# Kernel optimization log

Measured on AMD Instinct MI355X. Metric: run time of the kernel, lower is better.

Reference implementation:

```python
import jax, jax.numpy as jnp
import numpy as np

B, T, V, E, U = 1024, 128, 32000, 128, 512


def setup_inputs() -> dict:
    key = jax.random.key(0)
    ks = jax.random.split(key, 8)
    s = lambda k, *sh: jax.random.normal(k, sh, dtype=jnp.float32) * 0.05
    return {
        "tokens": jax.random.randint(ks[0], (B, T), 0, V, dtype=jnp.int32),
        "emb": s(ks[1], V, E),
        "Wx0": s(ks[2], E, U),
        "Wh0": s(ks[3], U, U),
        "b0": jnp.zeros((U,), jnp.float32),
        "Wx1": s(ks[4], U, U),
        "Wh1": s(ks[5], U, U),
        "b1": jnp.zeros((U,), jnp.float32),
        "Wo": s(ks[6], U, 1),
        "bo": jnp.zeros((1,), jnp.float32),
    }


def reference(tokens, emb, Wx0, Wh0, b0, Wx1, Wh1, b1, Wo, bo):
    # Embedding lookup: [B, T, E]
    x = emb[tokens]
    xs = jnp.swapaxes(x, 0, 1)  # [T, B, E] for time-major scan
    h0 = jnp.zeros((tokens.shape[0], Wh0.shape[0]), x.dtype)
    h1 = jnp.zeros((tokens.shape[0], Wh1.shape[0]), x.dtype)

    def step(carry, xt):
        h0, h1 = carry
        # SimpleRNNCell layer 0: h' = tanh(x@Wx + h@Wh + b)
        h0 = jnp.tanh(xt @ Wx0 + h0 @ Wh0 + b0)
        # SimpleRNNCell layer 1 stacked on out0
        h1 = jnp.tanh(h0 @ Wx1 + h1 @ Wh1 + b1)
        return (h0, h1), None

    (h0, h1), _ = jax.lax.scan(step, (h0, h1), xs)
    logits = h1 @ Wo + bo            # [B, 1]
    return jax.nn.sigmoid(logits)
```

## Files before the change

### kernel.cpp

```cpp
#include <hip/hip_runtime.h>
#include <hip/hip_bf16.h>

#define B_ 1024
#define T_ 128
#define E_ 128
#define U_ 512
#define V_ 32000
#define NC 16
#define NG 16
#define MB 64
#define NB 32
#define HS ((size_t)B_ * U_)

#define CTR_OFF 0
#define XMASK_OFF (512u << 10)
#define FH0_OFF (520u << 10)
#define FH1_OFF (528u << 10)
#define H0H_OFF (1u << 20)
#define H0L_OFF (4u << 20)
#define H1H_OFF (7u << 20)
#define H1L_OFF (9u << 20)
#define EMBW_OFF (11u << 20)
#define ZERO_BYTES (11u << 20)

typedef unsigned int uint32;
typedef __bf16 bf16x8 __attribute__((ext_vector_type(8)));
typedef float f32x4 __attribute__((ext_vector_type(4)));
typedef unsigned short us8 __attribute__((ext_vector_type(8)));

#define MFMA __builtin_amdgcn_mfma_f32_16x16x32_bf16

__device__ __forceinline__ unsigned short f2b(float f) {
  uint32 u = __builtin_bit_cast(uint32, f);
  u += 0x7fffu + ((u >> 16) & 1u);
  return (unsigned short)(u >> 16);
}
__device__ __forceinline__ float b2f(unsigned short h) {
  return __builtin_bit_cast(float, (uint32)h << 16);
}

__device__ __forceinline__ bf16x8 lds_frag(const unsigned short* s, int row, int k, int K) {
  uint32 off = (uint32)((row * K + k) * 2) ^ (uint32)((row & 7) << 4);
  us8 v = *(const us8*)((const char*)s + off);
  return __builtin_bit_cast(bf16x8, v);
}
__device__ __forceinline__ bf16x8 g_frag(const unsigned short* p) {
  us8 v = *(const us8*)p;
  return __builtin_bit_cast(bf16x8, v);
}
__device__ __forceinline__ void st_coh(unsigned short* p, unsigned short v) {
  __hip_atomic_store(p, v, __ATOMIC_RELAXED, __HIP_MEMORY_SCOPE_AGENT);
}
template <bool FAST>
__device__ __forceinline__ void st_h(unsigned short* p, unsigned short v) {
  if (FAST) *p = v; else st_coh(p, v);
}

template <bool FAST>
__device__ __forceinline__ void wave_signal(uint32* f, uint32 val, int lane) {
  asm volatile("s_waitcnt vmcnt(0)" ::: "memory");
  if (lane == 0) {
    if (FAST) *(volatile uint32*)f = val;
    else __hip_atomic_store(f, val, __ATOMIC_RELAXED, __HIP_MEMORY_SCOPE_AGENT);
  }
}

template <bool FAST, int DLT>
__device__ __forceinline__ void wave_wait(const uint32* f0, const uint32* f1,
                                          int t, int lane) {
  if (t == 0) return;
  const int t1 = t - DLT;
  const uint32 tgt = (lane < 16) ? (uint32)t
                                 : ((lane < 32 && t1 > 0) ? (uint32)t1 : 0u);
  const uint32* p = (lane < 16) ? (f0 + lane)
                                : ((lane < 32) ? (f1 + (lane & 15)) : f0);
  while (true) {
    uint32 v;
    if (FAST) v = *(const volatile uint32*)p;
    else v = __hip_atomic_load(p, __ATOMIC_RELAXED, __HIP_MEMORY_SCOPE_AGENT);
    if (__all(v >= tgt)) break;
    if (FAST) asm volatile("buffer_inv" ::: "memory");
    __builtin_amdgcn_s_sleep(2);
  }
  if (FAST) asm volatile("buffer_inv\n\ts_waitcnt vmcnt(0)" ::: "memory");
  else __builtin_amdgcn_fence(__ATOMIC_ACQUIRE, "agent");
}

__device__ __forceinline__ void bar_agent(uint32* ctr, int phase, int g, int tid) {
  asm volatile("s_waitcnt vmcnt(0)" ::: "memory");
  __syncthreads();
  if (tid == 0) {
    uint32* a = &ctr[(uint32)((phase << 4) | g) << 4];
    __hip_atomic_fetch_add(a, 1u, __ATOMIC_RELAXED, __HIP_MEMORY_SCOPE_AGENT);
    while (__hip_atomic_load(a, __ATOMIC_RELAXED, __HIP_MEMORY_SCOPE_AGENT) < NC)
      __builtin_amdgcn_s_sleep(1);
    __builtin_amdgcn_fence(__ATOMIC_ACQUIRE, "agent");
  }
  __syncthreads();
}

__global__ void rnn_init(unsigned char* ws) {
  const uint4 z = {0u, 0u, 0u, 0u};
  uint4* p = (uint4*)ws;
  size_t n = ZERO_BYTES / 16;
  for (size_t j = (size_t)blockIdx.x * blockDim.x + threadIdx.x; j < n;
       j += (size_t)gridDim.x * blockDim.x)
    p[j] = z;
}

__global__ __launch_bounds__(256) void embw_gemm(const float* __restrict__ emb,
                                                 const float* __restrict__ Wx0,
                                                 unsigned short* __restrict__ embW) {
  const int tid = threadIdx.x;
  const int lane = tid & 63;
  const int wv = tid >> 6;
  const int arow = lane & 15;
  const int kgrp = (lane >> 4) * 8;
  const int vrow = blockIdx.x * 64 + wv * 16;

  bf16x8 a[4];
  for (int kt = 0; kt < 4; ++kt) {
    const float* p = emb + (size_t)(vrow + arow) * E_ + kt * 32 + kgrp;
    float4 f0 = ((const float4*)p)[0];
    float4 f1 = ((const float4*)p)[1];
    us8 u;
    u[0] = f2b(f0.x); u[1] = f2b(f0.y); u[2] = f2b(f0.z); u[3] = f2b(f0.w);
    u[4] = f2b(f1.x); u[5] = f2b(f1.y); u[6] = f2b(f1.z); u[7] = f2b(f1.w);
    a[kt] = __builtin_bit_cast(bf16x8, u);
  }
  const int c0 = blockIdx.y * 64;
  for (int nt = 0; nt < 4; ++nt) {
    const int col = c0 + nt * 16 + (lane & 15);
    f32x4 acc = {0.f, 0.f, 0.f, 0.f};
    for (int kt = 0; kt < 4; ++kt) {
      us8 ub;
      for (int j = 0; j < 8; ++j)
        ub[j] = f2b(Wx0[(size_t)(kt * 32 + kgrp + j) * U_ + col]);
      acc = MFMA(a[kt], __builtin_bit_cast(bf16x8, ub), acc, 0, 0, 0);
    }
    const int crow = vrow + (lane >> 4) * 4;
    for (int i = 0; i < 4; ++i)
      embW[(size_t)(crow + i) * U_ + col] = f2b(acc[i]);
  }
}

template <bool FAST>
__device__ __forceinline__ void l0_loop(
    const int* __restrict__ tokens, const unsigned short* __restrict__ embW,
    unsigned short* h0h, unsigned short* h0l, const uint32* f0w,
    const uint32* f1w, uint32* myF0, const unsigned short* sWh0h,
    const unsigned short* sWh0l, int r0, int c0, int lane, int rowB, int kgrp,
    int rowA, float b0v0, float b0v1) {
  const int l15 = lane & 15;
  const float b0a[2] = {b0v0, b0v1};
  unsigned short embP[2][4];
#pragma unroll
  for (int nt = 0; nt < 2; ++nt)
    for (int i = 0; i < 4; ++i) {
      int tk = tokens[(size_t)(r0 + rowB + i) * T_ + 0];
      embP[nt][i] = embW[(size_t)tk * U_ + c0 + nt * 16 + l15];
    }

  for (int t = 0; t < T_; ++t) {
    wave_wait<FAST, 2>(f0w, f1w, t, lane);

    const size_t rb = (size_t)((t + 2) % 3) * HS;
    bf16x8 hh[16], hl[16];
    {
      const unsigned short* ph = h0h + rb + (size_t)rowA * U_ + kgrp;
      const unsigned short* pl = h0l + rb + (size_t)rowA * U_ + kgrp;
#pragma unroll
      for (int kt = 0; kt < 16; ++kt) {
        hh[kt] = g_frag(ph + kt * 32);
        hl[kt] = g_frag(pl + kt * 32);
      }
    }
    const size_t wb = (size_t)(t % 3) * HS;
#pragma unroll
    for (int nt = 0; nt < 2; ++nt) {
      const int colL = nt * 16 + l15;
      f32x4 aC, aD = {0.f, 0.f, 0.f, 0.f};
      for (int i = 0; i < 4; ++i) aC[i] = b0a[nt] + b2f(embP[nt][i]);
#pragma unroll
      for (int kt = 0; kt < 16; ++kt) {
        bf16x8 bh = lds_frag(sWh0h, colL, kt * 32 + kgrp, U_);
        bf16x8 bl = lds_frag(sWh0l, colL, kt * 32 + kgrp, U_);
        aC = MFMA(hh[kt], bh, aC, 0, 0, 0);
        aD = MFMA(hl[kt], bh, aD, 0, 0, 0);
        aD = MFMA(hh[kt], bl, aD, 0, 0, 0);
      }
      size_t ob = wb + (size_t)(r0 + rowB) * U_ + (c0 + colL);
      for (int i = 0; i < 4; ++i) {
        float v = tanhf(aC[i] + aD[i]);
        unsigned short hi = f2b(v);
        st_h<FAST>(&h0h[ob + (size_t)i * U_], hi);
        st_h<FAST>(&h0l[ob + (size_t)i * U_], f2b(v - b2f(hi)));
      }
    }
    wave_signal<FAST>(myF0, (uint32)(t + 1), lane);

    if (t + 1 < T_) {
#pragma unroll
      for (int nt = 0; nt < 2; ++nt)
        for (int i = 0; i < 4; ++i) {
          int tk = tokens[(size_t)(r0 + rowB + i) * T_ + (t + 1)];
          embP[nt][i] = embW[(size_t)tk * U_ + c0 + nt * 16 + l15];
        }
    }
  }
}

template <bool FAST>
__device__ __forceinline__ void l1_loop(
    unsigned short* h0h, unsigned short* h0l, unsigned short* h1h,
    unsigned short* h1l, const uint32* f0w, const uint32* f1w, uint32* myF1,
    const unsigned short* sWx1h, const unsigned short* sWh1h,
    const unsigned short* sWh1l, int r0, int c0, int lane, int rowB, int kgrp,
    int rowA, float b1v0, float b1v1) {
  const int l15 = lane & 15;
  const float b1a[2] = {b1v0, b1v1};

  for (int w = 1; w <= T_; ++w) {
    wave_wait<FAST, 1>(f0w, f1w, w, lane);

    f32x4 aB[2];
    {
      const size_t rb1 = (size_t)(w & 1) * HS;
      bf16x8 ah[16], al[16];
      const unsigned short* p1h = h1h + rb1 + (size_t)rowA * U_ + kgrp;
      const unsigned short* p1l = h1l + rb1 + (size_t)rowA * U_ + kgrp;
#pragma unroll
      for (int kt = 0; kt < 16; ++kt) {
        ah[kt] = g_frag(p1h + kt * 32);
        al[kt] = g_frag(p1l + kt * 32);
      }
#pragma unroll
      for (int nt = 0; nt < 2; ++nt) {
        const int colL = nt * 16 + l15;
        f32x4 acc = {b1a[nt], b1a[nt], b1a[nt], b1a[nt]};
#pragma unroll
        for (int kt = 0; kt < 16; ++kt) {
          bf16x8 bh = lds_frag(sWh1h, colL, kt * 32 + kgrp, U_);
          acc = MFMA(ah[kt], bh, acc, 0, 0, 0);
          acc = MFMA(al[kt], bh, acc, 0, 0, 0);
          if (kt < 15) {
            bf16x8 bl = lds_frag(sWh1l, colL, kt * 32 + kgrp, 480);
            acc = MFMA(ah[kt], bl, acc, 0, 0, 0);
          }
        }
        aB[nt] = acc;
      }
    }
    const size_t rb0 = (size_t)((w + 2) % 3) * HS;
    bf16x8 hh[16], hl[16];
    {
      const unsigned short* ph = h0h + rb0 + (size_t)rowA * U_ + kgrp;
      const unsigned short* pl = h0l + rb0 + (size_t)rowA * U_ + kgrp;
#pragma unroll
      for (int kt = 0; kt < 16; ++kt) {
        hh[kt] = g_frag(ph + kt * 32);
        hl[kt] = g_frag(pl + kt * 32);
      }
    }
    const size_t wb1 = (size_t)((w - 1) & 1) * HS;
#pragma unroll
    for (int nt = 0; nt < 2; ++nt) {
      const int colL = nt * 16 + l15;
      f32x4 aA = {0.f, 0.f, 0.f, 0.f};
#pragma unroll
      for (int kt = 0; kt < 16; ++kt) {
        bf16x8 bxh = lds_frag(sWx1h, colL, kt * 32 + kgrp, U_);
        aA = MFMA(hh[kt], bxh, aA, 0, 0, 0);
        aA = MFMA(hl[kt], bxh, aA, 0, 0, 0);
      }
      size_t ob = wb1 + (size_t)(r0 + rowB) * U_ + (c0 + colL);
      for (int i = 0; i < 4; ++i) {
        float v = tanhf(aA[i] + aB[nt][i]);
        unsigned short hi = f2b(v);
        st_h<FAST>(&h1h[ob + (size_t)i * U_], hi);
        st_h<FAST>(&h1l[ob + (size_t)i * U_], f2b(v - b2f(hi)));
      }
    }
    wave_signal<FAST>(myF1, (uint32)w, lane);
  }
}

__global__ __launch_bounds__(512, 2) void rnn_main(
    const int* __restrict__ tokens, const float* __restrict__ b0,
    const float* __restrict__ Wh0, const float* __restrict__ Wx1,
    const float* __restrict__ Wh1, const float* __restrict__ b1,
    unsigned char* ws) {
  __shared__ unsigned short sWh0h[NB * U_];
  __shared__ unsigned short sWh0l[NB * U_];
  __shared__ unsigned short sWx1h[NB * U_];
  __shared__ unsigned short sWh1h[NB * U_];
  __shared__ unsigned short sWh1l[NB * 480];
  __shared__ uint32 sFast;

  const int tid = threadIdx.x;
  const int bid = blockIdx.x;
  const int g = bid & (NG - 1);
  const int c = bid >> 4;
  const int r0 = g * MB;
  const int c0 = c * NB;

  uint32* ctr = (uint32*)(ws + CTR_OFF);
  uint32* fH0 = (uint32*)(ws + FH0_OFF);
  uint32* fH1 = (uint32*)(ws + FH1_OFF);
  unsigned short* h0h = (unsigned short*)(ws + H0H_OFF);
  unsigned short* h0l = (unsigned short*)(ws + H0L_OFF);
  unsigned short* h1h = (unsigned short*)(ws + H1H_OFF);
  unsigned short* h1l = (unsigned short*)(ws + H1L_OFF);
  const unsigned short* embW = (const unsigned short*)(ws + EMBW_OFF);

  for (int idx = tid; idx < NB * U_; idx += 512) {
    int cl = idx & 31, k = idx >> 5;
    float v = Wh0[(size_t)k * U_ + c0 + cl];
    unsigned short hi = f2b(v);
    uint32 off = (uint32)((cl * U_ + k) * 2) ^ (uint32)((cl & 7) << 4);
    *(unsigned short*)((char*)sWh0h + off) = hi;
    *(unsigned short*)((char*)sWh0l + off) = f2b(v - b2f(hi));
  }
  for (int idx = tid; idx < NB * U_; idx += 512) {
    int cl = idx & 31, k = idx >> 5;
    float v = Wx1[(size_t)k * U_ + c0 + cl];
    uint32 off = (uint32)((cl * U_ + k) * 2) ^ (uint32)((cl & 7) << 4);
    *(unsigned short*)((char*)sWx1h + off) = f2b(v);
  }
  for (int idx = tid; idx < NB * U_; idx += 512) {
    int cl = idx & 31, k = idx >> 5;
    float v = Wh1[(size_t)k * U_ + c0 + cl];
    unsigned short hi = f2b(v);
    uint32 off = (uint32)((cl * U_ + k) * 2) ^ (uint32)((cl & 7) << 4);
    *(unsigned short*)((char*)sWh1h + off) = hi;
    if (k < 480) {
      uint32 offl = (uint32)((cl * 480 + k) * 2) ^ (uint32)((cl & 7) << 4);
      *(unsigned short*)((char*)sWh1l + offl) = f2b(v - b2f(hi));
    }
  }

  {
    uint32 xcd;
    asm volatile("s_getreg_b32 %0, hwreg(HW_REG_XCC_ID)" : "=s"(xcd));
    uint32* xm = (uint32*)(ws + XMASK_OFF) + (uint32)g * 16;
    if (tid == 0)
      __hip_atomic_fetch_or(xm, 1u << (xcd & 31u), __ATOMIC_RELAXED,
                            __HIP_MEMORY_SCOPE_AGENT);
    bar_agent(ctr, T_, g, tid);
    if (tid == 0) {
      uint32 m = __hip_atomic_load(xm, __ATOMIC_RELAXED, __HIP_MEMORY_SCOPE_AGENT);
      sFast = (__popc(m) == 1) ? 1u : 0u;
    }
  }

  const int lane = tid & 63;
  const int wv = tid >> 6;
  const int mt = wv & 3;
  const int role = wv >> 2;
  const int l15 = lane & 15;
  const int rowB = mt * 16 + ((lane >> 4) << 2);
  const int kgrp = (lane >> 4) * 8;
  const int rowA = r0 + mt * 16 + l15;

  const uint32* f0w = fH0 + (((uint32)g * 4 + mt) << 4);
  const uint32* f1w = fH1 + (((uint32)g * 4 + mt) << 4);
  uint32* myF0 = (uint32*)f0w + c;
  uint32* myF1 = (uint32*)f1w + c;

  __syncthreads();
  const bool fast = (sFast != 0);

  if (role == 0) {
    const float b0v0 = b0[c0 + l15], b0v1 = b0[c0 + 16 + l15];
    if (fast)
      l0_loop<true>(tokens, embW, h0h, h0l, f0w, f1w, myF0, sWh0h, sWh0l, r0,
                    c0, lane, rowB, kgrp, rowA, b0v0, b0v1);
    else
      l0_loop<false>(tokens, embW, h0h, h0l, f0w, f1w, myF0, sWh0h, sWh0l, r0,
                     c0, lane, rowB, kgrp, rowA, b0v0, b0v1);
  } else {
    const float b1v0 = b1[c0 + l15], b1v1 = b1[c0 + 16 + l15];
    if (fast)
      l1_loop<true>(h0h, h0l, h1h, h1l, f0w, f1w, myF1, sWx1h, sWh1h, sWh1l,
                    r0, c0, lane, rowB, kgrp, rowA, b1v0, b1v1);
    else
      l1_loop<false>(h0h, h0l, h1h, h1l, f0w, f1w, myF1, sWx1h, sWh1h, sWh1l,
                     r0, c0, lane, rowB, kgrp, rowA, b1v0, b1v1);
  }
}

__global__ void rnn_final(const unsigned short* __restrict__ h1h,
                          const unsigned short* __restrict__ h1l,
                          const float* __restrict__ Wo,
                          const float* __restrict__ bo, float* __restrict__ out) {
  int lane = threadIdx.x & 63;
  int b = blockIdx.x * 4 + (threadIdx.x >> 6);
  us8 hh = *(const us8*)(h1h + (size_t)b * U_ + lane * 8);
  us8 hl = *(const us8*)(h1l + (size_t)b * U_ + lane * 8);
  const float4* wp = (const float4*)(Wo + lane * 8);
  float4 w0 = wp[0], w1 = wp[1];
  float s = (b2f(hh[0]) + b2f(hl[0])) * w0.x + (b2f(hh[1]) + b2f(hl[1])) * w0.y +
            (b2f(hh[2]) + b2f(hl[2])) * w0.z + (b2f(hh[3]) + b2f(hl[3])) * w0.w +
            (b2f(hh[4]) + b2f(hl[4])) * w1.x + (b2f(hh[5]) + b2f(hl[5])) * w1.y +
            (b2f(hh[6]) + b2f(hl[6])) * w1.z + (b2f(hh[7]) + b2f(hl[7])) * w1.w;
  for (int off = 32; off > 0; off >>= 1) s += __shfl_down(s, off, 64);
  if (lane == 0) out[b] = 1.0f / (1.0f + expf(-(s + bo[0])));
}

extern "C" void kernel_launch(void* const* d_in, const int* in_sizes, int n_in,
                              void* d_out, int out_size, void* d_ws, size_t ws_size,
                              hipStream_t stream) {
  const int* tokens = (const int*)d_in[0];
  const float* emb = (const float*)d_in[1];
  const float* Wx0 = (const float*)d_in[2];
  const float* Wh0 = (const float*)d_in[3];
  const float* b0 = (const float*)d_in[4];
  const float* Wx1 = (const float*)d_in[5];
  const float* Wh1 = (const float*)d_in[6];
  const float* b1 = (const float*)d_in[7];
  const float* Wo = (const float*)d_in[8];
  const float* bo = (const float*)d_in[9];
  unsigned char* ws = (unsigned char*)d_ws;
  float* out = (float*)d_out;

  hipLaunchKernelGGL(rnn_init, dim3(1024), dim3(256), 0, stream, ws);
  hipLaunchKernelGGL(embw_gemm, dim3(V_ / 64, U_ / 64), dim3(256), 0, stream,
                     emb, Wx0, (unsigned short*)(ws + EMBW_OFF));
  hipLaunchKernelGGL(rnn_main, dim3(NC * NG), dim3(512), 0, stream, tokens,
                     b0, Wh0, Wx1, Wh1, b1, ws);
  hipLaunchKernelGGL(rnn_final, dim3(256), dim3(256), 0, stream,
                     (const unsigned short*)(ws + H1H_OFF) + (size_t)1 * B_ * U_,
                     (const unsigned short*)(ws + H1L_OFF) + (size_t)1 * B_ * U_,
                     Wo, bo, out);
}
```

Before: 2.576 ms.

## Merge layer roles into per-column waves sharing h0 fragments across layers

The kernel used to give each wave either the layer-0 role or the layer-1 role, each covering two 16-column tiles. Now every wave handles one 16-column tile for both layers. It computes the h0 recurrence and the Wx1 projection from the same loaded h0 fragments, then runs the layer-1 step for the previous timestep. This avoids loading the h0 fragments twice and changes the flag layout to 32 per-wave flags, with separate pollers for layer 0 and layer 1. In exchange, layer 1 is now serialized inside the same wave, so the earlier overlap between layer-0 and layer-1 waves is lost, and each wave does more polling per step.

Result: faster. 2.313 ms (-10.2%).

```diff
diff --git a/kernel.cpp b/kernel.cpp
--- a/kernel.cpp
+++ b/kernel.cpp
@@ -57,23 +57,8 @@
 }
 
 template <bool FAST>
-__device__ __forceinline__ void wave_signal(uint32* f, uint32 val, int lane) {
-  asm volatile("s_waitcnt vmcnt(0)" ::: "memory");
-  if (lane == 0) {
-    if (FAST) *(volatile uint32*)f = val;
-    else __hip_atomic_store(f, val, __ATOMIC_RELAXED, __HIP_MEMORY_SCOPE_AGENT);
-  }
-}
-
-template <bool FAST, int DLT>
-__device__ __forceinline__ void wave_wait(const uint32* f0, const uint32* f1,
-                                          int t, int lane) {
-  if (t == 0) return;
-  const int t1 = t - DLT;
-  const uint32 tgt = (lane < 16) ? (uint32)t
-                                 : ((lane < 32 && t1 > 0) ? (uint32)t1 : 0u);
-  const uint32* p = (lane < 16) ? (f0 + lane)
-                                : ((lane < 32) ? (f1 + (lane & 15)) : f0);
+__device__ __forceinline__ void poll32(const uint32* base, uint32 tgt, int lane) {
+  const uint32* p = base + (lane & 31);
   while (true) {
     uint32 v;
     if (FAST) v = *(const volatile uint32*)p;
@@ -84,6 +69,15 @@
   }
   if (FAST) asm volatile("buffer_inv\n\ts_waitcnt vmcnt(0)" ::: "memory");
   else __builtin_amdgcn_fence(__ATOMIC_ACQUIRE, "agent");
+}
+
+template <bool FAST>
+__device__ __forceinline__ void signal(uint32* f, uint32 val, int lane) {
+  asm volatile("s_waitcnt vmcnt(0)" ::: "memory");
+  if (lane == 0) {
+    if (FAST) *(volatile uint32*)f = val;
+    else __hip_atomic_store(f, val, __ATOMIC_RELAXED, __HIP_MEMORY_SCOPE_AGENT);
+  }
 }
 
 __device__ __forceinline__ void bar_agent(uint32* ctr, int phase, int g, int tid) {
@@ -145,50 +139,89 @@
 }
 
 template <bool FAST>
-__device__ __forceinline__ void l0_loop(
+__device__ __forceinline__ void l1_step(
+    int t, f32x4 aA, unsigned short* h1h, unsigned short* h1l,
+    const uint32* f1w, uint32* myF1, const unsigned short* sWh1h,
+    const unsigned short* sWh1l, int r0, int c0, int lane, int colL, int rowB,
+    int kgrp, int rowA, float b1v) {
+  poll32<FAST>(f1w, (uint32)(t - 1), lane);
+  const size_t rb1 = (size_t)(t & 1) * HS;
+  bf16x8 ah[16], al[16];
+  {
+    const unsigned short* p1h = h1h + rb1 + (size_t)rowA * U_ + kgrp;
+    const unsigned short* p1l = h1l + rb1 + (size_t)rowA * U_ + kgrp;
+#pragma unroll
+    for (int kt = 0; kt < 16; ++kt) {
+      ah[kt] = g_frag(p1h + kt * 32);
+      al[kt] = g_frag(p1l + kt * 32);
+    }
+  }
+  f32x4 aB = {b1v, b1v, b1v, b1v};
+#pragma unroll
+  for (int kt = 0; kt < 16; ++kt) {
+    bf16x8 wh = lds_frag(sWh1h, colL, kt * 32 + kgrp, U_);
+    aB = MFMA(ah[kt], wh, aB, 0, 0, 0);
+    aB = MFMA(al[kt], wh, aB, 0, 0, 0);
+    if (kt < 15) {
+      bf16x8 wl = lds_frag(sWh1l, colL, kt * 32 + kgrp, 480);
+      aB = MFMA(ah[kt], wl, aB, 0, 0, 0);
+    }
+  }
+  const size_t wb1 = (size_t)((t - 1) & 1) * HS;
+  size_t ob = wb1 + (size_t)(r0 + rowB) * U_ + (c0 + colL);
+  for (int i = 0; i < 4; ++i) {
+    float v = tanhf(aA[i] + aB[i]);
+    unsigned short hi = f2b(v);
+    st_h<FAST>(&h1h[ob + (size_t)i * U_], hi);
+    st_h<FAST>(&h1l[ob + (size_t)i * U_], f2b(v - b2f(hi)));
+  }
+  signal<FAST>(myF1, (uint32)t, lane);
+}
+
+template <bool FAST>
+__device__ __forceinline__ void rnn_wave(
     const int* __restrict__ tokens, const unsigned short* __restrict__ embW,
-    unsigned short* h0h, unsigned short* h0l, const uint32* f0w,
-    const uint32* f1w, uint32* myF0, const unsigned short* sWh0h,
-    const unsigned short* sWh0l, int r0, int c0, int lane, int rowB, int kgrp,
-    int rowA, float b0v0, float b0v1) {
-  const int l15 = lane & 15;
-  const float b0a[2] = {b0v0, b0v1};
-  unsigned short embP[2][4];
-#pragma unroll
-  for (int nt = 0; nt < 2; ++nt)
-    for (int i = 0; i < 4; ++i) {
-      int tk = tokens[(size_t)(r0 + rowB + i) * T_ + 0];
-      embP[nt][i] = embW[(size_t)tk * U_ + c0 + nt * 16 + l15];
-    }
+    unsigned short* h0h, unsigned short* h0l, unsigned short* h1h,
+    unsigned short* h1l, const uint32* f0w, const uint32* f1w, uint32* myF0,
+    uint32* myF1, const unsigned short* sWh0h, const unsigned short* sWh0l,
+    const unsigned short* sWx1h, const unsigned short* sWh1h,
+    const unsigned short* sWh1l, int r0, int c0, int lane, int colL, int rowB,
+    int kgrp, int rowA, float b0v, float b1v) {
+  unsigned short embP[4];
+  for (int i = 0; i < 4; ++i) {
+    int tk = tokens[(size_t)(r0 + rowB + i) * T_ + 0];
+    embP[i] = embW[(size_t)tk * U_ + c0 + colL];
+  }
 
   for (int t = 0; t < T_; ++t) {
-    wave_wait<FAST, 2>(f0w, f1w, t, lane);
-
-    const size_t rb = (size_t)((t + 2) % 3) * HS;
+    if (t > 0) poll32<FAST>(f0w, (uint32)t, lane);
+    const size_t rb0 = (size_t)((t + 2) % 3) * HS;
     bf16x8 hh[16], hl[16];
     {
-      const unsigned short* ph = h0h + rb + (size_t)rowA * U_ + kgrp;
-      const unsigned short* pl = h0l + rb + (size_t)rowA * U_ + kgrp;
+      const unsigned short* ph = h0h + rb0 + (size_t)rowA * U_ + kgrp;
+      const unsigned short* pl = h0l + rb0 + (size_t)rowA * U_ + kgrp;
 #pragma unroll
       for (int kt = 0; kt < 16; ++kt) {
         hh[kt] = g_frag(ph + kt * 32);
         hl[kt] = g_frag(pl + kt * 32);
       }
     }
-    const size_t wb = (size_t)(t % 3) * HS;
-#pragma unroll
-    for (int nt = 0; nt < 2; ++nt) {
-      const int colL = nt * 16 + l15;
-      f32x4 aC, aD = {0.f, 0.f, 0.f, 0.f};
-      for (int i = 0; i < 4; ++i) aC[i] = b0a[nt] + b2f(embP[nt][i]);
-#pragma unroll
-      for (int kt = 0; kt < 16; ++kt) {
-        bf16x8 bh = lds_frag(sWh0h, colL, kt * 32 + kgrp, U_);
-        bf16x8 bl = lds_frag(sWh0l, colL, kt * 32 + kgrp, U_);
-        aC = MFMA(hh[kt], bh, aC, 0, 0, 0);
-        aD = MFMA(hl[kt], bh, aD, 0, 0, 0);
-        aD = MFMA(hh[kt], bl, aD, 0, 0, 0);
-      }
+    f32x4 aA = {0.f, 0.f, 0.f, 0.f};
+    f32x4 aC, aD = {0.f, 0.f, 0.f, 0.f};
+    for (int i = 0; i < 4; ++i) aC[i] = b0v + b2f(embP[i]);
+#pragma unroll
+    for (int kt = 0; kt < 16; ++kt) {
+      bf16x8 wx = lds_frag(sWx1h, colL, kt * 32 + kgrp, U_);
+      bf16x8 wh = lds_frag(sWh0h, colL, kt * 32 + kgrp, U_);
+      bf16x8 wl = lds_frag(sWh0l, colL, kt * 32 + kgrp, U_);
+      aA = MFMA(hh[kt], wx, aA, 0, 0, 0);
+      aA = MFMA(hl[kt], wx, aA, 0, 0, 0);
+      aC = MFMA(hh[kt], wh, aC, 0, 0, 0);
+      aD = MFMA(hl[kt], wh, aD, 0, 0, 0);
+      aD = MFMA(hh[kt], wl, aD, 0, 0, 0);
+    }
+    {
+      const size_t wb = (size_t)(t % 3) * HS;
       size_t ob = wb + (size_t)(r0 + rowB) * U_ + (c0 + colL);
       for (int i = 0; i < 4; ++i) {
         float v = tanhf(aC[i] + aD[i]);
@@ -197,61 +230,23 @@
         st_h<FAST>(&h0l[ob + (size_t)i * U_], f2b(v - b2f(hi)));
       }
     }
-    wave_signal<FAST>(myF0, (uint32)(t + 1), lane);
+    signal<FAST>(myF0, (uint32)(t + 1), lane);
 
     if (t + 1 < T_) {
-#pragma unroll
-      for (int nt = 0; nt < 2; ++nt)
-        for (int i = 0; i < 4; ++i) {
-          int tk = tokens[(size_t)(r0 + rowB + i) * T_ + (t + 1)];
-          embP[nt][i] = embW[(size_t)tk * U_ + c0 + nt * 16 + l15];
-        }
-    }
-  }
-}
-
-template <bool FAST>
-__device__ __forceinline__ void l1_loop(
-    unsigned short* h0h, unsigned short* h0l, unsigned short* h1h,
-    unsigned short* h1l, const uint32* f0w, const uint32* f1w, uint32* myF1,
-    const unsigned short* sWx1h, const unsigned short* sWh1h,
-    const unsigned short* sWh1l, int r0, int c0, int lane, int rowB, int kgrp,
-    int rowA, float b1v0, float b1v1) {
-  const int l15 = lane & 15;
-  const float b1a[2] = {b1v0, b1v1};
-
-  for (int w = 1; w <= T_; ++w) {
-    wave_wait<FAST, 1>(f0w, f1w, w, lane);
-
-    f32x4 aB[2];
-    {
-      const size_t rb1 = (size_t)(w & 1) * HS;
-      bf16x8 ah[16], al[16];
-      const unsigned short* p1h = h1h + rb1 + (size_t)rowA * U_ + kgrp;
-      const unsigned short* p1l = h1l + rb1 + (size_t)rowA * U_ + kgrp;
-#pragma unroll
-      for (int kt = 0; kt < 16; ++kt) {
-        ah[kt] = g_frag(p1h + kt * 32);
-        al[kt] = g_frag(p1l + kt * 32);
+      for (int i = 0; i < 4; ++i) {
+        int tk = tokens[(size_t)(r0 + rowB + i) * T_ + (t + 1)];
+        embP[i] = embW[(size_t)tk * U_ + c0 + colL];
       }
-#pragma unroll
-      for (int nt = 0; nt < 2; ++nt) {
-        const int colL = nt * 16 + l15;
-        f32x4 acc = {b1a[nt], b1a[nt], b1a[nt], b1a[nt]};
-#pragma unroll
-        for (int kt = 0; kt < 16; ++kt) {
-          bf16x8 bh = lds_frag(sWh1h, colL, kt * 32 + kgrp, U_);
-          acc = MFMA(ah[kt], bh, acc, 0, 0, 0);
-          acc = MFMA(al[kt], bh, acc, 0, 0, 0);
-          if (kt < 15) {
-            bf16x8 bl = lds_frag(sWh1l, colL, kt * 32 + kgrp, 480);
-            acc = MFMA(ah[kt], bl, acc, 0, 0, 0);
-          }
-        }
-        aB[nt] = acc;
-      }
-    }
-    const size_t rb0 = (size_t)((w + 2) % 3) * HS;
+    }
+
+    if (t >= 1)
+      l1_step<FAST>(t, aA, h1h, h1l, f1w, myF1, sWh1h, sWh1l, r0, c0, lane,
+                    colL, rowB, kgrp, rowA, b1v);
+  }
+
+  {
+    poll32<FAST>(f0w, (uint32)T_, lane);
+    const size_t rb0 = (size_t)((T_ + 2) % 3) * HS;
     bf16x8 hh[16], hl[16];
     {
       const unsigned short* ph = h0h + rb0 + (size_t)rowA * U_ + kgrp;
@@ -262,26 +257,15 @@
         hl[kt] = g_frag(pl + kt * 32);
       }
     }
-    const size_t wb1 = (size_t)((w - 1) & 1) * HS;
-#pragma unroll
-    for (int nt = 0; nt < 2; ++nt) {
-      const int colL = nt * 16 + l15;
-      f32x4 aA = {0.f, 0.f, 0.f, 0.f};
-#pragma unroll
-      for (int kt = 0; kt < 16; ++kt) {
-        bf16x8 bxh = lds_frag(sWx1h, colL, kt * 32 + kgrp, U_);
-        aA = MFMA(hh[kt], bxh, aA, 0, 0, 0);
-        aA = MFMA(hl[kt], bxh, aA, 0, 0, 0);
-      }
-      size_t ob = wb1 + (size_t)(r0 + rowB) * U_ + (c0 + colL);
-      for (int i = 0; i < 4; ++i) {
-        float v = tanhf(aA[i] + aB[nt][i]);
-        unsigned short hi = f2b(v);
-        st_h<FAST>(&h1h[ob + (size_t)i * U_], hi);
-        st_h<FAST>(&h1l[ob + (size_t)i * U_], f2b(v - b2f(hi)));
-      }
-    }
-    wave_signal<FAST>(myF1, (uint32)w, lane);
+    f32x4 aA = {0.f, 0.f, 0.f, 0.f};
+#pragma unroll
+    for (int kt = 0; kt < 16; ++kt) {
+      bf16x8 wx = lds_frag(sWx1h, colL, kt * 32 + kgrp, U_);
+      aA = MFMA(hh[kt], wx, aA, 0, 0, 0);
+      aA = MFMA(hl[kt], wx, aA, 0, 0, 0);
+    }
+    l1_step<FAST>(T_, aA, h1h, h1l, f1w, myF1, sWh1h, sWh1l, r0, c0, lane,
+                  colL, rowB, kgrp, rowA, b1v);
   }
 }
 
@@ -356,37 +340,31 @@
   const int lane = tid & 63;
   const int wv = tid >> 6;
   const int mt = wv & 3;
-  const int role = wv >> 2;
+  const int nt = wv >> 2;
   const int l15 = lane & 15;
+  const int colL = nt * 16 + l15;
   const int rowB = mt * 16 + ((lane >> 4) << 2);
   const int kgrp = (lane >> 4) * 8;
   const int rowA = r0 + mt * 16 + l15;
-
-  const uint32* f0w = fH0 + (((uint32)g * 4 + mt) << 4);
-  const uint32* f1w = fH1 + (((uint32)g * 4 + mt) << 4);
-  uint32* myF0 = (uint32*)f0w + c;
-  uint32* myF1 = (uint32*)f1w + c;
+  const float b0v = b0[c0 + colL];
+  const float b1v = b1[c0 + colL];
+
+  const uint32* f0w = fH0 + ((uint32)(g * 4 + mt) * 32);
+  const uint32* f1w = fH1 + ((uint32)(g * 4 + mt) * 32);
+  uint32* myF0 = (uint32*)f0w + (c * 2 + nt);
+  uint32* myF1 = (uint32*)f1w + (c * 2 + nt);
 
   __syncthreads();
   const bool fast = (sFast != 0);
 
-  if (role == 0) {
-    const float b0v0 = b0[c0 + l15], b0v1 = b0[c0 + 16 + l15];
-    if (fast)
-      l0_loop<true>(tokens, embW, h0h, h0l, f0w, f1w, myF0, sWh0h, sWh0l, r0,
-                    c0, lane, rowB, kgrp, rowA, b0v0, b0v1);
-    else
-      l0_loop<false>(tokens, embW, h0h, h0l, f0w, f1w, myF0, sWh0h, sWh0l, r0,
-                     c0, lane, rowB, kgrp, rowA, b0v0, b0v1);
-  } else {
-    const float b1v0 = b1[c0 + l15], b1v1 = b1[c0 + 16 + l15];
-    if (fast)
-      l1_loop<true>(h0h, h0l, h1h, h1l, f0w, f1w, myF1, sWx1h, sWh1h, sWh1l,
-                    r0, c0, lane, rowB, kgrp, rowA, b1v0, b1v1);
-    else
-      l1_loop<false>(h0h, h0l, h1h, h1l, f0w, f1w, myF1, sWx1h, sWh1h, sWh1l,
-                     r0, c0, lane, rowB, kgrp, rowA, b1v0, b1v1);
-  }
+  if (fast)
+    rnn_wave<true>(tokens, embW, h0h, h0l, h1h, h1l, f0w, f1w, myF0, myF1,
+                   sWh0h, sWh0l, sWx1h, sWh1h, sWh1l, r0, c0, lane, colL,
+                   rowB, kgrp, rowA, b0v, b1v);
+  else
+    rnn_wave<false>(tokens, embW, h0h, h0l, h1h, h1l, f0w, f1w, myF0, myF1,
+                    sWh0h, sWh0l, sWx1h, sWh1h, sWh1l, r0, c0, lane, colL,
+                    rowB, kgrp, rowA, b0v, b1v);
 }
 
 __global__ void rnn_final(const unsigned short* __restrict__ h1h,
```

## Split each wave's two column tiles across separate waves with 1024-thread blocks

Applied to the files above, without the earlier changes.

Doubles the block to 1024 threads so each wave computes a single 16-column tile instead of two, halving the serial MFMA chain per wave inside the recurrent step. Per-wave progress flags grow from 16 to 32 per row group, and the poll now checks 32 layer-0 and 32 layer-1 flags across the full 64 lanes. This cuts per-step latency on the critical path. In exchange, each wave now reloads the full h fragments for only half the work, which doubles global reads of h per block, and the block loses the 2-blocks-per-CU launch bound.

Result: slower. 5.469 ms (+112.3%).

```diff
diff --git a/kernel.cpp b/kernel.cpp
--- a/kernel.cpp
+++ b/kernel.cpp
@@ -57,23 +57,12 @@
 }
 
 template <bool FAST>
-__device__ __forceinline__ void wave_signal(uint32* f, uint32 val, int lane) {
-  asm volatile("s_waitcnt vmcnt(0)" ::: "memory");
-  if (lane == 0) {
-    if (FAST) *(volatile uint32*)f = val;
-    else __hip_atomic_store(f, val, __ATOMIC_RELAXED, __HIP_MEMORY_SCOPE_AGENT);
-  }
-}
-
-template <bool FAST, int DLT>
-__device__ __forceinline__ void wave_wait(const uint32* f0, const uint32* f1,
-                                          int t, int lane) {
-  if (t == 0) return;
-  const int t1 = t - DLT;
-  const uint32 tgt = (lane < 16) ? (uint32)t
-                                 : ((lane < 32 && t1 > 0) ? (uint32)t1 : 0u);
-  const uint32* p = (lane < 16) ? (f0 + lane)
-                                : ((lane < 32) ? (f1 + (lane & 15)) : f0);
+__device__ __forceinline__ void poll64(const uint32* f0, const uint32* f1,
+                                       int t0, int t1, int lane) {
+  if (t0 <= 0 && t1 <= 0) return;
+  const uint32 tgt = (lane < 32) ? (uint32)(t0 > 0 ? t0 : 0)
+                                 : (uint32)(t1 > 0 ? t1 : 0);
+  const uint32* p = (lane < 32) ? (f0 + lane) : (f1 + (lane & 31));
   while (true) {
     uint32 v;
     if (FAST) v = *(const volatile uint32*)p;
@@ -84,6 +73,15 @@
   }
   if (FAST) asm volatile("buffer_inv\n\ts_waitcnt vmcnt(0)" ::: "memory");
   else __builtin_amdgcn_fence(__ATOMIC_ACQUIRE, "agent");
+}
+
+template <bool FAST>
+__device__ __forceinline__ void signal(uint32* f, uint32 val, int lane) {
+  asm volatile("s_waitcnt vmcnt(0)" ::: "memory");
+  if (lane == 0) {
+    if (FAST) *(volatile uint32*)f = val;
+    else __hip_atomic_store(f, val, __ATOMIC_RELAXED, __HIP_MEMORY_SCOPE_AGENT);
+  }
 }
 
 __device__ __forceinline__ void bar_agent(uint32* ctr, int phase, int g, int tid) {
@@ -149,20 +147,16 @@
     const int* __restrict__ tokens, const unsigned short* __restrict__ embW,
     unsigned short* h0h, unsigned short* h0l, const uint32* f0w,
     const uint32* f1w, uint32* myF0, const unsigned short* sWh0h,
-    const unsigned short* sWh0l, int r0, int c0, int lane, int rowB, int kgrp,
-    int rowA, float b0v0, float b0v1) {
-  const int l15 = lane & 15;
-  const float b0a[2] = {b0v0, b0v1};
-  unsigned short embP[2][4];
-#pragma unroll
-  for (int nt = 0; nt < 2; ++nt)
-    for (int i = 0; i < 4; ++i) {
-      int tk = tokens[(size_t)(r0 + rowB + i) * T_ + 0];
-      embP[nt][i] = embW[(size_t)tk * U_ + c0 + nt * 16 + l15];
-    }
+    const unsigned short* sWh0l, int r0, int c0, int lane, int colL, int rowB,
+    int kgrp, int rowA, float b0v) {
+  unsigned short embP[4];
+  for (int i = 0; i < 4; ++i) {
+    int tk = tokens[(size_t)(r0 + rowB + i) * T_ + 0];
+    embP[i] = embW[(size_t)tk * U_ + c0 + colL];
+  }
 
   for (int t = 0; t < T_; ++t) {
-    wave_wait<FAST, 2>(f0w, f1w, t, lane);
+    poll64<FAST>(f0w, f1w, t, t - 2, lane);
 
     const size_t rb = (size_t)((t + 2) % 3) * HS;
     bf16x8 hh[16], hl[16];
@@ -175,37 +169,31 @@
         hl[kt] = g_frag(pl + kt * 32);
       }
     }
+    f32x4 aC, aD = {0.f, 0.f, 0.f, 0.f};
+    for (int i = 0; i < 4; ++i) aC[i] = b0v + b2f(embP[i]);
+#pragma unroll
+    for (int kt = 0; kt < 16; ++kt) {
+      bf16x8 bh = lds_frag(sWh0h, colL, kt * 32 + kgrp, U_);
+      bf16x8 bl = lds_frag(sWh0l, colL, kt * 32 + kgrp, U_);
+      aC = MFMA(hh[kt], bh, aC, 0, 0, 0);
+      aD = MFMA(hl[kt], bh, aD, 0, 0, 0);
+      aD = MFMA(hh[kt], bl, aD, 0, 0, 0);
+    }
     const size_t wb = (size_t)(t % 3) * HS;
-#pragma unroll
-    for (int nt = 0; nt < 2; ++nt) {
-      const int colL = nt * 16 + l15;
-      f32x4 aC, aD = {0.f, 0.f, 0.f, 0.f};
-      for (int i = 0; i < 4; ++i) aC[i] = b0a[nt] + b2f(embP[nt][i]);
-#pragma unroll
-      for (int kt = 0; kt < 16; ++kt) {
-        bf16x8 bh = lds_frag(sWh0h, colL, kt * 32 + kgrp, U_);
-        bf16x8 bl = lds_frag(sWh0l, colL, kt * 32 + kgrp, U_);
-        aC = MFMA(hh[kt], bh, aC, 0, 0, 0);
-        aD = MFMA(hl[kt], bh, aD, 0, 0, 0);
-        aD = MFMA(hh[kt], bl, aD, 0, 0, 0);
-      }
-      size_t ob = wb + (size_t)(r0 + rowB) * U_ + (c0 + colL);
+    size_t ob = wb + (size_t)(r0 + rowB) * U_ + (c0 + colL);
+    for (int i = 0; i < 4; ++i) {
+      float v = tanhf(aC[i] + aD[i]);
+      unsigned short hi = f2b(v);
+      st_h<FAST>(&h0h[ob + (size_t)i * U_], hi);
+      st_h<FAST>(&h0l[ob + (size_t)i * U_], f2b(v - b2f(hi)));
+    }
+    signal<FAST>(myF0, (uint32)(t + 1), lane);
+
+    if (t + 1 < T_) {
       for (int i = 0; i < 4; ++i) {
-        float v = tanhf(aC[i] + aD[i]);
-        unsigned short hi = f2b(v);
-        st_h<FAST>(&h0h[ob + (size_t)i * U_], hi);
-        st_h<FAST>(&h0l[ob + (size_t)i * U_], f2b(v - b2f(hi)));
-      }
-    }
-    wave_signal<FAST>(myF0, (uint32)(t + 1), lane);
-
-    if (t + 1 < T_) {
-#pragma unroll
-      for (int nt = 0; nt < 2; ++nt)
-        for (int i = 0; i < 4; ++i) {
-          int tk = tokens[(size_t)(r0 + rowB + i) * T_ + (t + 1)];
-          embP[nt][i] = embW[(size_t)tk * U_ + c0 + nt * 16 + l15];
-        }
+        int tk = tokens[(size_t)(r0 + rowB + i) * T_ + (t + 1)];
+        embP[i] = embW[(size_t)tk * U_ + c0 + colL];
+      }
     }
   }
 }
@@ -215,15 +203,12 @@
     unsigned short* h0h, unsigned short* h0l, unsigned short* h1h,
     unsigned short* h1l, const uint32* f0w, const uint32* f1w, uint32* myF1,
     const unsigned short* sWx1h, const unsigned short* sWh1h,
-    const unsigned short* sWh1l, int r0, int c0, int lane, int rowB, int kgrp,
-    int rowA, float b1v0, float b1v1) {
-  const int l15 = lane & 15;
-  const float b1a[2] = {b1v0, b1v1};
-
+    const unsigned short* sWh1l, int r0, int c0, int lane, int colL, int rowB,
+    int kgrp, int rowA, float b1v) {
   for (int w = 1; w <= T_; ++w) {
-    wave_wait<FAST, 1>(f0w, f1w, w, lane);
-
-    f32x4 aB[2];
+    poll64<FAST>(f0w, f1w, w, w - 1, lane);
+
+    f32x4 aB = {b1v, b1v, b1v, b1v};
     {
       const size_t rb1 = (size_t)(w & 1) * HS;
       bf16x8 ah[16], al[16];
@@ -235,25 +220,20 @@
         al[kt] = g_frag(p1l + kt * 32);
       }
 #pragma unroll
-      for (int nt = 0; nt < 2; ++nt) {
-        const int colL = nt * 16 + l15;
-        f32x4 acc = {b1a[nt], b1a[nt], b1a[nt], b1a[nt]};
-#pragma unroll
-        for (int kt = 0; kt < 16; ++kt) {
-          bf16x8 bh = lds_frag(sWh1h, colL, kt * 32 + kgrp, U_);
-          acc = MFMA(ah[kt], bh, acc, 0, 0, 0);
-          acc = MFMA(al[kt], bh, acc, 0, 0, 0);
-          if (kt < 15) {
-            bf16x8 bl = lds_frag(sWh1l, colL, kt * 32 + kgrp, 480);
-            acc = MFMA(ah[kt], bl, acc, 0, 0, 0);
-          }
+      for (int kt = 0; kt < 16; ++kt) {
+        bf16x8 bh = lds_frag(sWh1h, colL, kt * 32 + kgrp, U_);
+        aB = MFMA(ah[kt], bh, aB, 0, 0, 0);
+        aB = MFMA(al[kt], bh, aB, 0, 0, 0);
+        if (kt < 15) {
+          bf16x8 bl = lds_frag(sWh1l, colL, kt * 32 + kgrp, 480);
+          aB = MFMA(ah[kt], bl, aB, 0, 0, 0);
         }
-        aB[nt] = acc;
-      }
-    }
-    const size_t rb0 = (size_t)((w + 2) % 3) * HS;
-    bf16x8 hh[16], hl[16];
+      }
+    }
+    f32x4 aA = {0.f, 0.f, 0.f, 0.f};
     {
+      const size_t rb0 = (size_t)((w + 2) % 3) * HS;
+      bf16x8 hh[16], hl[16];
       const unsigned short* ph = h0h + rb0 + (size_t)rowA * U_ + kgrp;
       const unsigned short* pl = h0l + rb0 + (size_t)rowA * U_ + kgrp;
 #pragma unroll
@@ -261,31 +241,26 @@
         hh[kt] = g_frag(ph + kt * 32);
         hl[kt] = g_frag(pl + kt * 32);
       }
-    }
-    const size_t wb1 = (size_t)((w - 1) & 1) * HS;
-#pragma unroll
-    for (int nt = 0; nt < 2; ++nt) {
-      const int colL = nt * 16 + l15;
-      f32x4 aA = {0.f, 0.f, 0.f, 0.f};
 #pragma unroll
       for (int kt = 0; kt < 16; ++kt) {
         bf16x8 bxh = lds_frag(sWx1h, colL, kt * 32 + kgrp, U_);
         aA = MFMA(hh[kt], bxh, aA, 0, 0, 0);
         aA = MFMA(hl[kt], bxh, aA, 0, 0, 0);
       }
-      size_t ob = wb1 + (size_t)(r0 + rowB) * U_ + (c0 + colL);
-      for (int i = 0; i < 4; ++i) {
-        float v = tanhf(aA[i] + aB[nt][i]);
-        unsigned short hi = f2b(v);
-        st_h<FAST>(&h1h[ob + (size_t)i * U_], hi);
-        st_h<FAST>(&h1l[ob + (size_t)i * U_], f2b(v - b2f(hi)));
-      }
-    }
-    wave_signal<FAST>(myF1, (uint32)w, lane);
-  }
-}
-
-__global__ __launch_bounds__(512, 2) void rnn_main(
+    }
+    const size_t wb1 = (size_t)((w - 1) & 1) * HS;
+    size_t ob = wb1 + (size_t)(r0 + rowB) * U_ + (c0 + colL);
+    for (int i = 0; i < 4; ++i) {
+      float v = tanhf(aA[i] + aB[i]);
+      unsigned short hi = f2b(v);
+      st_h<FAST>(&h1h[ob + (size_t)i * U_], hi);
+      st_h<FAST>(&h1l[ob + (size_t)i * U_], f2b(v - b2f(hi)));
+    }
+    signal<FAST>(myF1, (uint32)w, lane);
+  }
+}
+
+__global__ __launch_bounds__(1024) void rnn_main(
     const int* __restrict__ tokens, const float* __restrict__ b0,
     const float* __restrict__ Wh0, const float* __restrict__ Wx1,
     const float* __restrict__ Wh1, const float* __restrict__ b1,
@@ -313,7 +288,7 @@
   unsigned short* h1l = (unsigned short*)(ws + H1L_OFF);
   const unsigned short* embW = (const unsigned short*)(ws + EMBW_OFF);
 
-  for (int idx = tid; idx < NB * U_; idx += 512) {
+  for (int idx = tid; idx < NB * U_; idx += 1024) {
     int cl = idx & 31, k = idx >> 5;
     float v = Wh0[(size_t)k * U_ + c0 + cl];
     unsigned short hi = f2b(v);
@@ -321,13 +296,13 @@
     *(unsigned short*)((char*)sWh0h + off) = hi;
     *(unsigned short*)((char*)sWh0l + off) = f2b(v - b2f(hi));
   }
-  for (int idx = tid; idx < NB * U_; idx += 512) {
+  for (int idx = tid; idx < NB * U_; idx += 1024) {
     int cl = idx & 31, k = idx >> 5;
     float v = Wx1[(size_t)k * U_ + c0 + cl];
     uint32 off = (uint32)((cl * U_ + k) * 2) ^ (uint32)((cl & 7) << 4);
     *(unsigned short*)((char*)sWx1h + off) = f2b(v);
   }
-  for (int idx = tid; idx < NB * U_; idx += 512) {
+  for (int idx = tid; idx < NB * U_; idx += 1024) {
     int cl = idx & 31, k = idx >> 5;
     float v = Wh1[(size_t)k * U_ + c0 + cl];
     unsigned short hi = f2b(v);
@@ -356,36 +331,38 @@
   const int lane = tid & 63;
   const int wv = tid >> 6;
   const int mt = wv & 3;
-  const int role = wv >> 2;
+  const int nt = (wv >> 2) & 1;
+  const int role = wv >> 3;
   const int l15 = lane & 15;
+  const int colL = nt * 16 + l15;
   const int rowB = mt * 16 + ((lane >> 4) << 2);
   const int kgrp = (lane >> 4) * 8;
   const int rowA = r0 + mt * 16 + l15;
 
-  const uint32* f0w = fH0 + (((uint32)g * 4 + mt) << 4);
-  const uint32* f1w = fH1 + (((uint32)g * 4 + mt) << 4);
-  uint32* myF0 = (uint32*)f0w + c;
-  uint32* myF1 = (uint32*)f1w + c;
+  const uint32* f0w = fH0 + ((uint32)(g * 4 + mt) * 32);
+  const uint32* f1w = fH1 + ((uint32)(g * 4 + mt) * 32);
+  uint32* myF0 = (uint32*)f0w + (c * 2 + nt);
+  uint32* myF1 = (uint32*)f1w + (c * 2 + nt);
 
   __syncthreads();
   const bool fast = (sFast != 0);
 
   if (role == 0) {
-    const float b0v0 = b0[c0 + l15], b0v1 = b0[c0 + 16 + l15];
+    const float b0v = b0[c0 + colL];
     if (fast)
       l0_loop<true>(tokens, embW, h0h, h0l, f0w, f1w, myF0, sWh0h, sWh0l, r0,
-                    c0, lane, rowB, kgrp, rowA, b0v0, b0v1);
+                    c0, lane, colL, rowB, kgrp, rowA, b0v);
     else
       l0_loop<false>(tokens, embW, h0h, h0l, f0w, f1w, myF0, sWh0h, sWh0l, r0,
-                     c0, lane, rowB, kgrp, rowA, b0v0, b0v1);
+                     c0, lane, colL, rowB, kgrp, rowA, b0v);
   } else {
-    const float b1v0 = b1[c0 + l15], b1v1 = b1[c0 + 16 + l15];
+    const float b1v = b1[c0 + colL];
     if (fast)
       l1_loop<true>(h0h, h0l, h1h, h1l, f0w, f1w, myF1, sWx1h, sWh1h, sWh1l,
-                    r0, c0, lane, rowB, kgrp, rowA, b1v0, b1v1);
+                    r0, c0, lane, colL, rowB, kgrp, rowA, b1v);
     else
       l1_loop<false>(h0h, h0l, h1h, h1l, f0w, f1w, myF1, sWx1h, sWh1h, sWh1l,
-                     r0, c0, lane, rowB, kgrp, rowA, b1v0, b1v1);
+                     r0, c0, lane, colL, rowB, kgrp, rowA, b1v);
   }
 }
 
@@ -426,7 +403,7 @@
   hipLaunchKernelGGL(rnn_init, dim3(1024), dim3(256), 0, stream, ws);
   hipLaunchKernelGGL(embw_gemm, dim3(V_ / 64, U_ / 64), dim3(256), 0, stream,
                      emb, Wx0, (unsigned short*)(ws + EMBW_OFF));
-  hipLaunchKernelGGL(rnn_main, dim3(NC * NG), dim3(512), 0, stream, tokens,
+  hipLaunchKernelGGL(rnn_main, dim3(NC * NG), dim3(1024), 0, stream, tokens,
                      b0, Wh0, Wx1, Wh1, b1, ws);
   hipLaunchKernelGGL(rnn_final, dim3(256), dim3(256), 0, stream,
                      (const unsigned short*)(ws + H1H_OFF) + (size_t)1 * B_ * U_,
```
